# Optimization experiments

Measured on AMD Instinct MI355X. Metric: run time of the kernel, lower is better.

Reference implementation:

```python
import jax, jax.numpy as jnp
import numpy as np

EPS = 1e-08


def _similarity_transform(S1, S2):
    """Batched Procrustes: S1, S2 are [B, 3, N]. Returns aligned S1_hat [B, 3, N]."""
    mu1 = jnp.mean(S1, axis=-1, keepdims=True)          # [B,3,1]
    mu2 = jnp.mean(S2, axis=-1, keepdims=True)
    X1 = S1 - mu1
    X2 = S2 - mu2
    var1 = jnp.sum(X1 * X1, axis=(1, 2))                # [B]
    # cross-covariance K = X1 @ X2^T + eps (eps added to every entry, as in torch ref)
    K = jnp.einsum('bin,bjn->bij', X1, X2) + EPS        # [B,3,3]
    U, s, Vh = jnp.linalg.svd(K, full_matrices=False)
    V = jnp.swapaxes(Vh, -1, -2)
    # det(U @ V^T) = det(U @ Vh); sign has zero gradient, same as torch
    sign = jax.lax.stop_gradient(jnp.sign(jnp.linalg.det(jnp.matmul(U, Vh))))  # [B]
    ones = jnp.ones_like(sign)
    d = jnp.stack([ones, ones, sign], axis=-1)          # diag of Z, [B,3]
    # R = V @ Z @ U^T
    R = jnp.einsum('bik,bk,bjk->bij', V, d, U)          # [B,3,3]
    scale = jnp.einsum('bij,bji->b', R, K) / var1       # trace(R@K)/var1, [B]
    t = mu2 - scale[:, None, None] * jnp.matmul(R, mu1)  # [B,3,1]
    S1_hat = scale[:, None, None] * jnp.matmul(R, S1) + t
    return S1_hat


def setup_inputs() -> dict:
    key = jax.random.key(0)
    k1, k2 = jax.random.split(key)
    B, N = 1024, 6890
    pred = jax.random.normal(k1, (B, N, 3), dtype=jnp.float32)
    gt = jax.random.normal(k2, (B, N, 3), dtype=jnp.float32)
    return {"pred": pred, "gt": gt}


def reference(pred, gt):
    # inputs are [B, N, 3] -> torch code transposes to [B, 3, N] and back
    S1 = jnp.swapaxes(pred, 1, 2)
    S2 = jnp.swapaxes(gt, 1, 2)
    S1_hat = jnp.swapaxes(_similarity_transform(S1, S2), 1, 2)  # [B,N,3]
    # loss_type == 'l1', reduction='none'
    return jnp.abs(S1_hat - gt)
```

## Files before the change

### kernel.cpp

```cpp
#include <hip/hip_runtime.h>
#include <math.h>

#define NPTS 6890
#define BATCH 1024
#define FLOATS_PER_BATCH (NPTS * 3)
#define NGROUPS 1722

__device__ __forceinline__ void accum(float* acc, float p0, float p1, float p2,
                                      float g0, float g1, float g2) {
  acc[0] += p0;  acc[1] += p1;  acc[2] += p2;
  acc[3] += g0;  acc[4] += g1;  acc[5] += g2;
  acc[6] += p0 * p0 + p1 * p1 + p2 * p2;
  acc[7]  += p0 * g0;  acc[8]  += p0 * g1;  acc[9]  += p0 * g2;
  acc[10] += p1 * g0;  acc[11] += p1 * g1;  acc[12] += p1 * g2;
  acc[13] += p2 * g0;  acc[14] += p2 * g1;  acc[15] += p2 * g2;
}

__global__ __launch_bounds__(256) void reduce_kernel(
    const float* __restrict__ pred, const float* __restrict__ gt,
    float* __restrict__ sums) {
  const int b = blockIdx.x;
  const size_t ofs0 = (size_t)b * FLOATS_PER_BATCH;
  const int skip = (b & 1) ? 2 : 0;
  const size_t ofs = ofs0 + (size_t)skip * 3;
  const float4* __restrict__ p4 = (const float4*)(pred + ofs);
  const float4* __restrict__ g4 = (const float4*)(gt + ofs);

  float acc[16];
#pragma unroll
  for (int i = 0; i < 16; ++i) acc[i] = 0.f;

  for (int gi = threadIdx.x; gi < NGROUPS; gi += 256) {
    const float4 a0 = p4[3 * gi], a1 = p4[3 * gi + 1], a2 = p4[3 * gi + 2];
    const float4 c0 = g4[3 * gi], c1 = g4[3 * gi + 1], c2 = g4[3 * gi + 2];
    accum(acc, a0.x, a0.y, a0.z, c0.x, c0.y, c0.z);
    accum(acc, a0.w, a1.x, a1.y, c0.w, c1.x, c1.y);
    accum(acc, a1.z, a1.w, a2.x, c1.z, c1.w, c2.x);
    accum(acc, a2.y, a2.z, a2.w, c2.y, c2.z, c2.w);
  }

  if (threadIdx.x < 2) {
    const int n = skip ? (int)threadIdx.x : (NPTS - 2 + (int)threadIdx.x);
    const float* pp = pred + ofs0 + 3 * n;
    const float* gg = gt + ofs0 + 3 * n;
    accum(acc, pp[0], pp[1], pp[2], gg[0], gg[1], gg[2]);
  }

#pragma unroll
  for (int i = 0; i < 16; ++i) {
#pragma unroll
    for (int off = 32; off > 0; off >>= 1)
      acc[i] += __shfl_down(acc[i], off, 64);
  }

  __shared__ float red[4][16];
  const int wave = threadIdx.x >> 6;
  const int lane = threadIdx.x & 63;
  if (lane == 0) {
#pragma unroll
    for (int i = 0; i < 16; ++i) red[wave][i] = acc[i];
  }
  __syncthreads();
  if (threadIdx.x < 16) {
    const int i = threadIdx.x;
    sums[b * 16 + i] = red[0][i] + red[1][i] + red[2][i] + red[3][i];
  }
}

__global__ void solve_kernel(const float* __restrict__ sums,
                             float* __restrict__ params) {
  const int b = blockIdx.x * blockDim.x + threadIdx.x;
  if (b >= BATCH) return;
  const float* s = sums + b * 16;
  const double Ninv = 1.0 / (double)NPTS;

  double sp[3] = {s[0], s[1], s[2]};
  double sg[3] = {s[3], s[4], s[5]};
  double mu1[3], mu2[3];
#pragma unroll
  for (int i = 0; i < 3; ++i) { mu1[i] = sp[i] * Ninv; mu2[i] = sg[i] * Ninv; }
  const double var1 =
      (double)s[6] - (sp[0] * sp[0] + sp[1] * sp[1] + sp[2] * sp[2]) * Ninv;

  double K[3][3];
#pragma unroll
  for (int i = 0; i < 3; ++i)
#pragma unroll
    for (int j = 0; j < 3; ++j)
      K[i][j] = (double)s[7 + 3 * i + j] - sp[i] * sg[j] * Ninv + 1e-8;

  double A[3][3];
#pragma unroll
  for (int i = 0; i < 3; ++i)
#pragma unroll
    for (int j = 0; j < 3; ++j)
      A[i][j] = K[0][i] * K[0][j] + K[1][i] * K[1][j] + K[2][i] * K[2][j];

  double V[3][3] = {{1, 0, 0}, {0, 1, 0}, {0, 0, 1}};
  for (int sweep = 0; sweep < 30; ++sweep) {
    const double off = A[0][1] * A[0][1] + A[0][2] * A[0][2] + A[1][2] * A[1][2];
    const double nrm = A[0][0] + A[1][1] + A[2][2];
    if (off <= 1e-30 * nrm * nrm) break;
    for (int pq = 0; pq < 3; ++pq) {
      const int p = (pq == 2) ? 1 : 0;
      const int q = (pq == 0) ? 1 : 2;
      const double apq = A[p][q];
      if (apq == 0.0) continue;
      const double theta = (A[q][q] - A[p][p]) / (2.0 * apq);
      const double tt =
          ((theta >= 0.0) ? 1.0 : -1.0) / (fabs(theta) + sqrt(theta * theta + 1.0));
      const double c = 1.0 / sqrt(tt * tt + 1.0);
      const double sn = tt * c;
      const double app = A[p][p], aqq = A[q][q];
      A[p][p] = app - tt * apq;
      A[q][q] = aqq + tt * apq;
      A[p][q] = 0.0; A[q][p] = 0.0;
      const int r = 3 - p - q;
      const double arp = A[r][p], arq = A[r][q];
      A[r][p] = c * arp - sn * arq; A[p][r] = A[r][p];
      A[r][q] = sn * arp + c * arq; A[q][r] = A[r][q];
#pragma unroll
      for (int k = 0; k < 3; ++k) {
        const double vkp = V[k][p], vkq = V[k][q];
        V[k][p] = c * vkp - sn * vkq;
        V[k][q] = sn * vkp + c * vkq;
      }
    }
  }

  double w[3] = {A[0][0], A[1][1], A[2][2]};
  int i0 = 0, i1 = 1, i2 = 2, tmp;
  if (w[i0] < w[i1]) { tmp = i0; i0 = i1; i1 = tmp; }
  if (w[i0] < w[i2]) { tmp = i0; i0 = i2; i2 = tmp; }
  if (w[i1] < w[i2]) { tmp = i1; i1 = i2; i2 = tmp; }
  const double sv0 = sqrt(fmax(w[i0], 0.0));
  const double sv1 = sqrt(fmax(w[i1], 0.0));
  const double sv2 = sqrt(fmax(w[i2], 0.0));

  const double detK =
      K[0][0] * (K[1][1] * K[2][2] - K[1][2] * K[2][1]) -
      K[0][1] * (K[1][0] * K[2][2] - K[1][2] * K[2][0]) +
      K[0][2] * (K[1][0] * K[2][1] - K[1][1] * K[2][0]);
  const double sgn = (detK > 0.0) ? 1.0 : ((detK < 0.0) ? -1.0 : 0.0);

  const double floor0 = sv0 * 1e-12 + 1e-300;
  const double z0 = 1.0 / fmax(sv0, floor0);
  const double z1 = 1.0 / fmax(sv1, floor0);
  const double z2 = sgn / fmax(sv2, floor0);

  double W[3][3];
#pragma unroll
  for (int a = 0; a < 3; ++a)
#pragma unroll
    for (int c = 0; c < 3; ++c)
      W[a][c] = V[a][i0] * V[c][i0] * z0 + V[a][i1] * V[c][i1] * z1 +
                V[a][i2] * V[c][i2] * z2;

  double R[3][3];
#pragma unroll
  for (int a = 0; a < 3; ++a)
#pragma unroll
    for (int c = 0; c < 3; ++c)
      R[a][c] = W[a][0] * K[c][0] + W[a][1] * K[c][1] + W[a][2] * K[c][2];

  const double trace = sv0 + sv1 + sgn * sv2;
  const double scale = trace / var1;

  float* pr = params + b * 12;
#pragma unroll
  for (int a = 0; a < 3; ++a) {
#pragma unroll
    for (int c = 0; c < 3; ++c) pr[3 * a + c] = (float)(scale * R[a][c]);
    pr[9 + a] = (float)(mu2[a] - scale * (R[a][0] * mu1[0] + R[a][1] * mu1[1] +
                                          R[a][2] * mu1[2]));
  }
}

__device__ __forceinline__ void xform(const float* m, float p0, float p1,
                                      float p2, float g0, float g1, float g2,
                                      float& o0, float& o1, float& o2) {
  o0 = fabsf(m[0] * p0 + m[1] * p1 + m[2] * p2 + m[9] - g0);
  o1 = fabsf(m[3] * p0 + m[4] * p1 + m[5] * p2 + m[10] - g1);
  o2 = fabsf(m[6] * p0 + m[7] * p1 + m[8] * p2 + m[11] - g2);
}

__global__ __launch_bounds__(256) void apply_kernel(
    const float* __restrict__ pred, const float* __restrict__ gt,
    const float* __restrict__ params, float* __restrict__ out) {
  const int b = blockIdx.y;
  float m[12];
#pragma unroll
  for (int i = 0; i < 12; ++i) m[i] = params[b * 12 + i];

  const size_t ofs0 = (size_t)b * FLOATS_PER_BATCH;
  const int skip = (b & 1) ? 2 : 0;
  const size_t ofs = ofs0 + (size_t)skip * 3;
  const int gi = blockIdx.x * 256 + threadIdx.x;

  if (gi < NGROUPS) {
    const float4* __restrict__ p4 = (const float4*)(pred + ofs);
    const float4* __restrict__ g4 = (const float4*)(gt + ofs);
    float4* __restrict__ o4 = (float4*)(out + ofs);
    const float4 a0 = p4[3 * gi], a1 = p4[3 * gi + 1], a2 = p4[3 * gi + 2];
    const float4 c0 = g4[3 * gi], c1 = g4[3 * gi + 1], c2 = g4[3 * gi + 2];
    float4 r0, r1, r2;
    xform(m, a0.x, a0.y, a0.z, c0.x, c0.y, c0.z, r0.x, r0.y, r0.z);
    xform(m, a0.w, a1.x, a1.y, c0.w, c1.x, c1.y, r0.w, r1.x, r1.y);
    xform(m, a1.z, a1.w, a2.x, c1.z, c1.w, c2.x, r1.z, r1.w, r2.x);
    xform(m, a2.y, a2.z, a2.w, c2.y, c2.z, c2.w, r2.y, r2.z, r2.w);
    o4[3 * gi] = r0; o4[3 * gi + 1] = r1; o4[3 * gi + 2] = r2;
  }

  if (blockIdx.x == 0 && threadIdx.x < 2) {
    const int n = skip ? (int)threadIdx.x : (NPTS - 2 + (int)threadIdx.x);
    const float* pp = pred + ofs0 + 3 * n;
    const float* gg = gt + ofs0 + 3 * n;
    float* oo = out + ofs0 + 3 * n;
    xform(m, pp[0], pp[1], pp[2], gg[0], gg[1], gg[2], oo[0], oo[1], oo[2]);
  }
}

extern "C" void kernel_launch(void* const* d_in, const int* in_sizes, int n_in,
                              void* d_out, int out_size, void* d_ws, size_t ws_size,
                              hipStream_t stream) {
  const float* pred = (const float*)d_in[0];
  const float* gt   = (const float*)d_in[1];
  float* out = (float*)d_out;
  float* sums   = (float*)d_ws;
  float* params = sums + BATCH * 16;

  hipLaunchKernelGGL(reduce_kernel, dim3(BATCH), dim3(256), 0, stream,
                     pred, gt, sums);
  hipLaunchKernelGGL(solve_kernel, dim3((BATCH + 255) / 256), dim3(256), 0,
                     stream, sums, params);
  hipLaunchKernelGGL(apply_kernel, dim3((NGROUPS + 255) / 256, BATCH),
                     dim3(256), 0, stream, pred, gt, params, out);
}
```

Baseline: 244.7 us.

## Split per-batch reduction into two chunks with unrolled loads and lighter wave reduction

The reduce kernel now runs two blocks per batch, each handling a fixed, fully unrolled set of float4 groups. Each thread issues its loads up front to raise memory-level parallelism, and the partial sums are combined in double precision inside the solve kernel. The wave reduction is cut to two xor shuffles plus a padded shared-memory tree, and the solve kernel launches with 64-thread blocks to spread across more CUs. The cost is twice the partial-sum traffic and a hardcoded group layout that only fits NGROUPS=1722.

```diff
diff --git a/kernel.cpp b/kernel.cpp
--- a/kernel.cpp
+++ b/kernel.cpp
@@ -5,6 +5,7 @@
 #define BATCH 1024
 #define FLOATS_PER_BATCH (NPTS * 3)
 #define NGROUPS 1722
+#define CHUNKS 2
 
 __device__ __forceinline__ void accum(float* acc, float p0, float p1, float p2,
                                       float g0, float g1, float g2) {
@@ -16,31 +17,63 @@
   acc[13] += p2 * g0;  acc[14] += p2 * g1;  acc[15] += p2 * g2;
 }
 
-__global__ __launch_bounds__(256) void reduce_kernel(
+__device__ __forceinline__ void accum_group(float* acc,
+                                            const float4& a0, const float4& a1,
+                                            const float4& a2, const float4& e0,
+                                            const float4& e1, const float4& e2) {
+  accum(acc, a0.x, a0.y, a0.z, e0.x, e0.y, e0.z);
+  accum(acc, a0.w, a1.x, a1.y, e0.w, e1.x, e1.y);
+  accum(acc, a1.z, a1.w, a2.x, e1.z, e1.w, e2.x);
+  accum(acc, a2.y, a2.z, a2.w, e2.y, e2.z, e2.w);
+}
+
+__global__ __launch_bounds__(256, 4) void reduce_kernel(
     const float* __restrict__ pred, const float* __restrict__ gt,
-    float* __restrict__ sums) {
+    float* __restrict__ partial) {
   const int b = blockIdx.x;
+  const int c = blockIdx.y;
   const size_t ofs0 = (size_t)b * FLOATS_PER_BATCH;
   const int skip = (b & 1) ? 2 : 0;
   const size_t ofs = ofs0 + (size_t)skip * 3;
-  const float4* __restrict__ p4 = (const float4*)(pred + ofs);
-  const float4* __restrict__ g4 = (const float4*)(gt + ofs);
+  const float4* __restrict__ P = (const float4*)(pred + ofs);
+  const float4* __restrict__ G = (const float4*)(gt + ofs);
 
   float acc[16];
 #pragma unroll
   for (int i = 0; i < 16; ++i) acc[i] = 0.f;
 
-  for (int gi = threadIdx.x; gi < NGROUPS; gi += 256) {
-    const float4 a0 = p4[3 * gi], a1 = p4[3 * gi + 1], a2 = p4[3 * gi + 2];
-    const float4 c0 = g4[3 * gi], c1 = g4[3 * gi + 1], c2 = g4[3 * gi + 2];
-    accum(acc, a0.x, a0.y, a0.z, c0.x, c0.y, c0.z);
-    accum(acc, a0.w, a1.x, a1.y, c0.w, c1.x, c1.y);
-    accum(acc, a1.z, a1.w, a2.x, c1.z, c1.w, c2.x);
-    accum(acc, a2.y, a2.z, a2.w, c2.y, c2.z, c2.w);
-  }
-
-  if (threadIdx.x < 2) {
-    const int n = skip ? (int)threadIdx.x : (NPTS - 2 + (int)threadIdx.x);
+  const int t = (int)threadIdx.x;
+  const int g1 = c * 256 + t;
+  const int g2 = g1 + 512;
+
+  {
+    const float4 a0 = P[3 * g1], a1 = P[3 * g1 + 1], a2 = P[3 * g1 + 2];
+    const float4 b0 = P[3 * g2], b1 = P[3 * g2 + 1], b2 = P[3 * g2 + 2];
+    const float4 e0 = G[3 * g1], e1 = G[3 * g1 + 1], e2 = G[3 * g1 + 2];
+    const float4 f0 = G[3 * g2], f1 = G[3 * g2 + 1], f2 = G[3 * g2 + 2];
+    accum_group(acc, a0, a1, a2, e0, e1, e2);
+    accum_group(acc, b0, b1, b2, f0, f1, f2);
+  }
+
+  const int g3 = g1 + 1024;
+  if (c == 0) {
+    const int g4 = t + 1536;
+    const bool v4 = g4 < NGROUPS;
+    const int g4c = v4 ? g4 : g3;
+    const float4 a0 = P[3 * g3], a1 = P[3 * g3 + 1], a2 = P[3 * g3 + 2];
+    const float4 b0 = P[3 * g4c], b1 = P[3 * g4c + 1], b2 = P[3 * g4c + 2];
+    const float4 e0 = G[3 * g3], e1 = G[3 * g3 + 1], e2 = G[3 * g3 + 2];
+    const float4 f0 = G[3 * g4c], f1 = G[3 * g4c + 1], f2 = G[3 * g4c + 2];
+    accum_group(acc, a0, a1, a2, e0, e1, e2);
+    if (v4) accum_group(acc, b0, b1, b2, f0, f1, f2);
+  } else {
+    const float4 a0 = P[3 * g3], a1 = P[3 * g3 + 1], a2 = P[3 * g3 + 2];
+    const float4 e0 = G[3 * g3], e1 = G[3 * g3 + 1], e2 = G[3 * g3 + 2];
+    accum_group(acc, a0, a1, a2, e0, e1, e2);
+  }
+
+  if (c == 0 && t < 2) {
+    const int n = skip ? t : (NPTS - 2 + t);
     const float* pp = pred + ofs0 + 3 * n;
     const float* gg = gt + ofs0 + 3 * n;
     accum(acc, pp[0], pp[1], pp[2], gg[0], gg[1], gg[2]);
@@ -48,30 +81,37 @@
 
 #pragma unroll
   for (int i = 0; i < 16; ++i) {
-#pragma unroll
-    for (int off = 32; off > 0; off >>= 1)
-      acc[i] += __shfl_down(acc[i], off, 64);
-  }
-
-  __shared__ float red[4][16];
-  const int wave = threadIdx.x >> 6;
-  const int lane = threadIdx.x & 63;
-  if (lane == 0) {
-#pragma unroll
-    for (int i = 0; i < 16; ++i) red[wave][i] = acc[i];
+    acc[i] += __shfl_xor(acc[i], 16, 64);
+    acc[i] += __shfl_xor(acc[i], 32, 64);
+  }
+  __shared__ float red[4][16][17];
+  const int wave = t >> 6;
+  const int lane = t & 63;
+  if (lane < 16) {
+#pragma unroll
+    for (int i = 0; i < 16; ++i) red[wave][lane][i] = acc[i];
   }
   __syncthreads();
-  if (threadIdx.x < 16) {
-    const int i = threadIdx.x;
-    sums[b * 16 + i] = red[0][i] + red[1][i] + red[2][i] + red[3][i];
-  }
-}
-
-__global__ void solve_kernel(const float* __restrict__ sums,
+  if (t < 16) {
+    float s = 0.f;
+#pragma unroll
+    for (int w = 0; w < 4; ++w)
+#pragma unroll
+      for (int r = 0; r < 16; ++r) s += red[w][r][t];
+    partial[(b * CHUNKS + c) * 16 + t] = s;
+  }
+}
+
+__global__ void solve_kernel(const float* __restrict__ partial,
                              float* __restrict__ params) {
   const int b = blockIdx.x * blockDim.x + threadIdx.x;
   if (b >= BATCH) return;
-  const float* s = sums + b * 16;
+  const float* ps = partial + b * (CHUNKS * 16);
+  double s[16];
+#pragma unroll
+  for (int i = 0; i < 16; ++i)
+    s[i] = (double)ps[i] + (double)ps[16 + i];
+
   const double Ninv = 1.0 / (double)NPTS;
 
   double sp[3] = {s[0], s[1], s[2]};
@@ -80,14 +120,14 @@
 #pragma unroll
   for (int i = 0; i < 3; ++i) { mu1[i] = sp[i] * Ninv; mu2[i] = sg[i] * Ninv; }
   const double var1 =
-      (double)s[6] - (sp[0] * sp[0] + sp[1] * sp[1] + sp[2] * sp[2]) * Ninv;
+      s[6] - (sp[0] * sp[0] + sp[1] * sp[1] + sp[2] * sp[2]) * Ninv;
 
   double K[3][3];
 #pragma unroll
   for (int i = 0; i < 3; ++i)
 #pragma unroll
     for (int j = 0; j < 3; ++j)
-      K[i][j] = (double)s[7 + 3 * i + j] - sp[i] * sg[j] * Ninv + 1e-8;
+      K[i][j] = s[7 + 3 * i + j] - sp[i] * sg[j] * Ninv + 1e-8;
 
   double A[3][3];
 #pragma unroll
@@ -109,21 +149,21 @@
       const double theta = (A[q][q] - A[p][p]) / (2.0 * apq);
       const double tt =
           ((theta >= 0.0) ? 1.0 : -1.0) / (fabs(theta) + sqrt(theta * theta + 1.0));
-      const double c = 1.0 / sqrt(tt * tt + 1.0);
-      const double sn = tt * c;
+      const double cc = 1.0 / sqrt(tt * tt + 1.0);
+      const double sn = tt * cc;
       const double app = A[p][p], aqq = A[q][q];
       A[p][p] = app - tt * apq;
       A[q][q] = aqq + tt * apq;
       A[p][q] = 0.0; A[q][p] = 0.0;
       const int r = 3 - p - q;
       const double arp = A[r][p], arq = A[r][q];
-      A[r][p] = c * arp - sn * arq; A[p][r] = A[r][p];
-      A[r][q] = sn * arp + c * arq; A[q][r] = A[r][q];
+      A[r][p] = cc * arp - sn * arq; A[p][r] = A[r][p];
+      A[r][q] = sn * arp + cc * arq; A[q][r] = A[r][q];
 #pragma unroll
       for (int k = 0; k < 3; ++k) {
         const double vkp = V[k][p], vkq = V[k][q];
-        V[k][p] = c * vkp - sn * vkq;
-        V[k][q] = sn * vkp + c * vkq;
+        V[k][p] = cc * vkp - sn * vkq;
+        V[k][q] = sn * vkp + cc * vkq;
       }
     }
   }
@@ -226,13 +266,13 @@
   const float* pred = (const float*)d_in[0];
   const float* gt   = (const float*)d_in[1];
   float* out = (float*)d_out;
-  float* sums   = (float*)d_ws;
-  float* params = sums + BATCH * 16;
-
-  hipLaunchKernelGGL(reduce_kernel, dim3(BATCH), dim3(256), 0, stream,
-                     pred, gt, sums);
-  hipLaunchKernelGGL(solve_kernel, dim3((BATCH + 255) / 256), dim3(256), 0,
-                     stream, sums, params);
+  float* partial = (float*)d_ws;
+  float* params  = partial + BATCH * CHUNKS * 16;
+
+  hipLaunchKernelGGL(reduce_kernel, dim3(BATCH, CHUNKS), dim3(256), 0, stream,
+                     pred, gt, partial);
+  hipLaunchKernelGGL(solve_kernel, dim3((BATCH + 63) / 64), dim3(64), 0,
+                     stream, partial, params);
   hipLaunchKernelGGL(apply_kernel, dim3((NGROUPS + 255) / 256, BATCH),
                      dim3(256), 0, stream, pred, gt, params, out);
 }
```

Measured after the change: 249.3 us. Within noise of the previous version (+1.9%).
